# Kernel tuning notes

Hardware: AMD Instinct MI355X
Metric: run time of the kernel (lower is better)

Reference implementation:

```python
import jax, jax.numpy as jnp
import numpy as np

HEADS = 16
DIM_HEAD = 64


def setup_inputs() -> dict:
    key = jax.random.key(0)
    k1, k2, k3, k4 = jax.random.split(key, 4)
    B, T, D = 4, 1024, 1024
    x = jax.random.normal(k1, (B, T, D), dtype=jnp.float32)
    w_qkv = jax.random.normal(k2, (3 * HEADS * DIM_HEAD, D), dtype=jnp.float32) * (1.0 / np.sqrt(D))
    w_out = jax.random.normal(k3, (D, HEADS * DIM_HEAD), dtype=jnp.float32) * (1.0 / np.sqrt(HEADS * DIM_HEAD))
    rel_bias = jax.random.normal(k4, (2 * 1024 - 1, HEADS), dtype=jnp.float32) * 0.02
    return {"x": x, "w_qkv": w_qkv, "w_out": w_out, "rel_bias": rel_bias}


def reference(x, w_qkv, w_out, rel_bias):
    b, t, _ = x.shape
    h, dh = HEADS, DIM_HEAD
    scale = dh ** (-0.5)
    qkv = x @ w_qkv.T  # [b, t, 3*h*dh]
    # einops 'b t (d k h) -> k b h t d': last axis factors as (dh, 3, h)
    qkv = qkv.reshape(b, t, dh, 3, h).transpose(3, 0, 4, 1, 2)  # [3, b, h, t, dh]
    q, k, v = qkv[0], qkv[1], qkv[2]
    scores = jnp.einsum('bhid,bhjd->bhij', q, k) * scale  # [b, h, t, t]
    # relative position bias: rel[i,j] = j - i + t - 1
    rel = jnp.arange(t)[None, :] - jnp.arange(t)[:, None] + (t - 1)  # [t, t]
    bias = rel_bias[rel]  # [t, t, h]
    scores = scores + bias.transpose(2, 0, 1)[None]  # [b, h, t, t]
    attn = jax.nn.softmax(scores, axis=-1)
    out = jnp.einsum('bhij,bhjd->bhid', attn, v)  # [b, h, t, dh]
    out = out.transpose(0, 2, 1, 3).reshape(b, t, h * dh)  # 'b h t d -> b t (h d)'
    return out @ w_out.T
```

## Files before the change

### kernel.cpp

```cpp
#include <hip/hip_runtime.h>
#include <hip/hip_bf16.h>

typedef short bf16x8 __attribute__((ext_vector_type(8)));
typedef float f32x4  __attribute__((ext_vector_type(4)));

typedef __attribute__((address_space(3))) void lds_t;
typedef __attribute__((address_space(1))) void gbl_t;

#define MFMA16(a,b,c) __builtin_amdgcn_mfma_f32_16x16x32_bf16((a),(b),(c),0,0,0)

__device__ __forceinline__ unsigned short f2bf(float f) {
    __hip_bfloat16 h = __float2bfloat16(f);
    return __builtin_bit_cast(unsigned short, h);
}
__device__ __forceinline__ float bf2f(unsigned short u) {
    __hip_bfloat16 h = __builtin_bit_cast(__hip_bfloat16, u);
    return __bfloat162float(h);
}

__global__ void prep_hi_rows(const float* __restrict__ src,
                             unsigned short* __restrict__ dst, int total4) {
    for (int idx = blockIdx.x * blockDim.x + threadIdx.x; idx < total4;
         idx += gridDim.x * blockDim.x) {
        int base = idx * 4;
        float4 v = *reinterpret_cast<const float4*>(src + base);
        ushort4 hi;
        hi.x = f2bf(v.x);
        hi.y = f2bf(v.y);
        hi.z = f2bf(v.z);
        hi.w = f2bf(v.w);
        *reinterpret_cast<ushort4*>(dst + base) = hi;
    }
}

__global__ void prep_hi_wqkv(const float* __restrict__ w,
                             unsigned short* __restrict__ dst) {
    for (int idx = blockIdx.x * blockDim.x + threadIdx.x; idx < 3072 * 256;
         idx += gridDim.x * blockDim.x) {
        int base = idx * 4;
        int n = base >> 10, c = base & 1023;
        int d = n & 63, which = n >> 10, h = (n >> 6) & 15;
        int srow = d * 48 + which * 16 + h;
        float4 v = *reinterpret_cast<const float4*>(w + (size_t)srow * 1024 + c);
        ushort4 hi;
        hi.x = f2bf(v.x);
        hi.y = f2bf(v.y);
        hi.z = f2bf(v.z);
        hi.w = f2bf(v.w);
        *reinterpret_cast<ushort4*>(dst + (size_t)n * 1024 + c) = hi;
    }
}

__global__ __launch_bounds__(512, 2) void gemm256_hi(
    const unsigned short* __restrict__ A, const unsigned short* __restrict__ B,
    unsigned short* __restrict__ outQ, unsigned short* __restrict__ outK,
    unsigned short* __restrict__ outV) {
    __shared__ unsigned short lds[65536];
    const int tid = threadIdx.x;
    const int wid = tid >> 6, lane = tid & 63;
    const int lrow = lane & 15, lgrp = lane >> 4;
    const int wr = wid >> 2, wc = wid & 3;
    const int mtile = blockIdx.y * 256, ntile = blockIdx.x * 256;

    const int csw = lgrp ^ ((lrow >> 1) & 3);
    const int aoff = (wr * 128 + lrow) * 32 + csw * 8;
    const int boff = 32768 + (wc * 64 + lrow) * 32 + csw * 8;

    const int sreg = wid * 2;
    const int srow0 = sreg * 16 + (lane >> 2);
    const int srow1 = (sreg + 1) * 16 + (lane >> 2);
    const int schunk = (lane & 3) ^ ((lane >> 3) & 3);
    const int sdst0 = sreg * 512;

    f32x4 acc[8][4];
#pragma unroll
    for (int i = 0; i < 8; ++i)
#pragma unroll
        for (int j = 0; j < 4; ++j) {
            f32x4 z = {0.f, 0.f, 0.f, 0.f};
            acc[i][j] = z;
        }

#pragma unroll
    for (int s0 = 0; s0 < 2; ++s0) {
        const int kb = s0 * 32;
        __builtin_amdgcn_global_load_lds(
            (const gbl_t*)(A + (size_t)(mtile + srow0) * 1024 + kb + schunk * 8),
            (lds_t*)(lds + s0 * 8192 + sdst0), 16, 0, 0);
        __builtin_amdgcn_global_load_lds(
            (const gbl_t*)(A + (size_t)(mtile + srow1) * 1024 + kb + schunk * 8),
            (lds_t*)(lds + s0 * 8192 + sdst0 + 512), 16, 0, 0);
        __builtin_amdgcn_global_load_lds(
            (const gbl_t*)(B + (size_t)(ntile + srow0) * 1024 + kb + schunk * 8),
            (lds_t*)(lds + 32768 + s0 * 8192 + sdst0), 16, 0, 0);
        __builtin_amdgcn_global_load_lds(
            (const gbl_t*)(B + (size_t)(ntile + srow1) * 1024 + kb + schunk * 8),
            (lds_t*)(lds + 32768 + s0 * 8192 + sdst0 + 512), 16, 0, 0);
    }
    asm volatile("s_waitcnt vmcnt(4)" ::: "memory");
    __syncthreads();

    for (int s = 0; s < 32; ++s) {
        const int sa = s & 3;
        const unsigned short* sbase = lds + sa * 8192;

        bf16x8 af[8];
#pragma unroll
        for (int i = 0; i < 8; ++i)
            af[i] = *reinterpret_cast<const bf16x8*>(sbase + aoff + i * 512);
        bf16x8 b0 = *reinterpret_cast<const bf16x8*>(sbase + boff);
        bf16x8 b1 = *reinterpret_cast<const bf16x8*>(sbase + boff + 512);

        if (s <= 29) {
            const int kb2 = (s + 2) * 32;
            const int s2 = (s + 2) & 3;
            __builtin_amdgcn_global_load_lds(
                (const gbl_t*)(A + (size_t)(mtile + srow0) * 1024 + kb2 + schunk * 8),
                (lds_t*)(lds + s2 * 8192 + sdst0), 16, 0, 0);
            __builtin_amdgcn_global_load_lds(
                (const gbl_t*)(A + (size_t)(mtile + srow1) * 1024 + kb2 + schunk * 8),
                (lds_t*)(lds + s2 * 8192 + sdst0 + 512), 16, 0, 0);
        }
        __builtin_amdgcn_s_setprio(1);
#pragma unroll
        for (int i = 0; i < 8; ++i) {
            acc[i][0] = MFMA16(af[i], b0, acc[i][0]);
            acc[i][1] = MFMA16(af[i], b1, acc[i][1]);
        }
        __builtin_amdgcn_s_setprio(0);

        bf16x8 b2 = *reinterpret_cast<const bf16x8*>(sbase + boff + 1024);
        bf16x8 b3 = *reinterpret_cast<const bf16x8*>(sbase + boff + 1536);
        if (s <= 29) {
            const int kb2 = (s + 2) * 32;
            const int s2 = (s + 2) & 3;
            __builtin_amdgcn_global_load_lds(
                (const gbl_t*)(B + (size_t)(ntile + srow0) * 1024 + kb2 + schunk * 8),
                (lds_t*)(lds + 32768 + s2 * 8192 + sdst0), 16, 0, 0);
            __builtin_amdgcn_global_load_lds(
                (const gbl_t*)(B + (size_t)(ntile + srow1) * 1024 + kb2 + schunk * 8),
                (lds_t*)(lds + 32768 + s2 * 8192 + sdst0 + 512), 16, 0, 0);
        }
        __builtin_amdgcn_s_setprio(1);
#pragma unroll
        for (int i = 0; i < 8; ++i) {
            acc[i][2] = MFMA16(af[i], b2, acc[i][2]);
            acc[i][3] = MFMA16(af[i], b3, acc[i][3]);
        }
        __builtin_amdgcn_s_setprio(0);

        if (s < 31) {
            if (s <= 29)
                asm volatile("s_waitcnt vmcnt(4)" ::: "memory");
            else
                asm volatile("s_waitcnt vmcnt(0)" ::: "memory");
            __syncthreads();
        }
    }

#pragma unroll
    for (int i = 0; i < 8; ++i) {
#pragma unroll
        for (int j = 0; j < 4; ++j) {
#pragma unroll
            for (int r = 0; r < 4; ++r) {
                float v = acc[i][j][r];
                int m = mtile + wr * 128 + i * 16 + lgrp * 4 + r;
                int n = ntile + wc * 64 + j * 16 + lrow;
                int which = n >> 10;
                int hh = (n >> 6) & 15;
                int d = n & 63;
                int b = m >> 10, t = m & 1023;
                unsigned short* dstp =
                    (which == 0) ? outQ : ((which == 1) ? outK : outV);
                dstp[((size_t)((b << 4) + hh) * 1024 + t) * 64 + d] = f2bf(v);
            }
        }
    }
}

__global__ __launch_bounds__(256, 3) void gemm_out_v4(
    const unsigned short* __restrict__ A, const unsigned short* __restrict__ B,
    float* __restrict__ outF) {
    __shared__ unsigned short As[4][64 * 32];
    __shared__ unsigned short Bs[4][128 * 32];
    const int tid = threadIdx.x;
    const int wid = tid >> 6, lane = tid & 63;
    const int lrow = lane & 15, lgrp = lane >> 4;
    const int wr = wid >> 1, wc = wid & 1;
    const int h = blockIdx.x;
    const int xcd = h & 7, within = h >> 3;
    const int mtile = (xcd * 8 + (within & 7)) * 64;
    const int ntile = (within >> 3) * 128;

    const int csw = lgrp ^ ((lrow >> 1) & 3);
    const int aoff = (wr * 32 + lrow) * 32 + csw * 8;
    const int boff = (wc * 64 + lrow) * 32 + csw * 8;

    const int srow = tid >> 2;
    const int schunk = (tid & 3) ^ ((tid >> 3) & 3);
    const unsigned short* Arow = A + (size_t)(mtile + srow) * 1024 + schunk * 8;
    const unsigned short* Brow0 = B + (size_t)(ntile + srow) * 1024 + schunk * 8;
    const unsigned short* Brow1 =
        B + (size_t)(ntile + 64 + srow) * 1024 + schunk * 8;

    f32x4 acc[2][4];
#pragma unroll
    for (int i = 0; i < 2; ++i)
#pragma unroll
        for (int j = 0; j < 4; ++j) {
            f32x4 z = {0.f, 0.f, 0.f, 0.f};
            acc[i][j] = z;
        }

#pragma unroll
    for (int s0 = 0; s0 < 2; ++s0) {
        const int kb = s0 * 32;
        __builtin_amdgcn_global_load_lds((const gbl_t*)(Arow + kb),
                                         (lds_t*)(&As[s0][0] + tid * 8), 16, 0,
                                         0);
        __builtin_amdgcn_global_load_lds((const gbl_t*)(Brow0 + kb),
                                         (lds_t*)(&Bs[s0][0] + tid * 8), 16, 0,
                                         0);
        __builtin_amdgcn_global_load_lds((const gbl_t*)(Brow1 + kb),
                                         (lds_t*)(&Bs[s0][0] + 2048 + tid * 8),
                                         16, 0, 0);
    }
    asm volatile("s_waitcnt vmcnt(3)" ::: "memory");
    __syncthreads();

    for (int s = 0; s < 32; ++s) {
        const int sa = s & 3;
        if (s <= 29) {
            const int kb = (s + 2) * 32;
            const int s2 = (s + 2) & 3;
            __builtin_amdgcn_global_load_lds((const gbl_t*)(Arow + kb),
                                             (lds_t*)(&As[s2][0] + tid * 8), 16,
                                             0, 0);
            __builtin_amdgcn_global_load_lds((const gbl_t*)(Brow0 + kb),
                                             (lds_t*)(&Bs[s2][0] + tid * 8), 16,
                                             0, 0);
            __builtin_amdgcn_global_load_lds(
                (const gbl_t*)(Brow1 + kb),
                (lds_t*)(&Bs[s2][0] + 2048 + tid * 8), 16, 0, 0);
        }
        bf16x8 af[2], bfv[4];
#pragma unroll
        for (int i = 0; i < 2; ++i)
            af[i] = *reinterpret_cast<const bf16x8*>(&As[sa][0] + aoff + i * 512);
#pragma unroll
        for (int j = 0; j < 4; ++j)
            bfv[j] =
                *reinterpret_cast<const bf16x8*>(&Bs[sa][0] + boff + j * 512);
        __builtin_amdgcn_s_setprio(1);
#pragma unroll
        for (int i = 0; i < 2; ++i)
#pragma unroll
            for (int j = 0; j < 4; ++j)
                acc[i][j] = MFMA16(af[i], bfv[j], acc[i][j]);
        __builtin_amdgcn_s_setprio(0);
        if (s < 31) {
            if (s <= 29)
                asm volatile("s_waitcnt vmcnt(3)" ::: "memory");
            else
                asm volatile("s_waitcnt vmcnt(0)" ::: "memory");
            __syncthreads();
        }
    }

#pragma unroll
    for (int i = 0; i < 2; ++i)
#pragma unroll
        for (int j = 0; j < 4; ++j)
#pragma unroll
            for (int r = 0; r < 4; ++r) {
                int m = mtile + wr * 32 + i * 16 + lgrp * 4 + r;
                int n = ntile + wc * 64 + j * 16 + lrow;
                outF[(size_t)m * 1024 + n] = acc[i][j][r];
            }
}

__global__ __launch_bounds__(256) void transpose_v(
    const unsigned short* __restrict__ Vb, unsigned short* __restrict__ Vtg) {
    __shared__ unsigned short L[64][72];
    const int tt = blockIdx.x, bh = blockIdx.y;
    const int tid = threadIdx.x;
#pragma unroll
    for (int e = 0; e < 2; ++e) {
        int chunk = e * 256 + tid;
        int r = chunk >> 3, c = (chunk & 7) * 8;
        uint4 v = *reinterpret_cast<const uint4*>(
            Vb + ((size_t)bh * 1024 + tt * 64 + r) * 64 + c);
        *reinterpret_cast<uint4*>(&L[r][c]) = v;
    }
    __syncthreads();
#pragma unroll
    for (int e = 0; e < 2; ++e) {
        int chunk = e * 256 + tid;
        int d = chunk >> 3, t0 = (chunk & 7) * 8;
        unsigned short tmp[8];
#pragma unroll
        for (int u = 0; u < 8; ++u) tmp[u] = L[t0 + u][d];
        *reinterpret_cast<uint4*>(Vtg + ((size_t)bh * 64 + d) * 1024 + tt * 64 +
                                  t0) = *reinterpret_cast<const uint4*>(tmp);
    }
}

__global__ __launch_bounds__(512) void attn_kernel(
    const unsigned short* __restrict__ Qb, const unsigned short* __restrict__ Kb,
    const unsigned short* __restrict__ Vtg, const float* __restrict__ rel_bias,
    unsigned short* __restrict__ A3) {
    const int qt = blockIdx.x;
    const int bh = blockIdx.y;
    const int b = bh >> 4, h = bh & 15;
    const int tid = threadIdx.x;
    const int w = tid >> 6, lane = tid & 63;
    const int lrow = lane & 15, lgrp = lane >> 4;
    const float LOG2E = 1.4426950408889634f;
    const float SCALE2 = 0.125f * 1.4426950408889634f;
    const float THR = 11.5f;

    __shared__ unsigned short Ks[2][64 * 64];
    __shared__ unsigned short Vs[2][64 * 64];
    __shared__ unsigned short Ps[8][16 * 64];
    __shared__ float Bias2[2][192];

    const unsigned short* Ktile = Kb + (size_t)bh * 1024 * 64;
    const unsigned short* Vtile = Vtg + (size_t)bh * 64 * 1024;

    const unsigned short* Qp =
        Qb + ((size_t)bh * 1024 + qt * 128 + w * 16 + lrow) * 64;
    bf16x8 qa0 = *reinterpret_cast<const bf16x8*>(Qp + lgrp * 8);
    bf16x8 qa1 = *reinterpret_cast<const bf16x8*>(Qp + 32 + lgrp * 8);

    const int sr0 = w * 8 + (lane >> 3);
    const int sc_lo = lane & 7;

    float m_run = -3.0e38f;
    float l_run = 0.f;
    f32x4 o_acc[4];
#pragma unroll
    for (int n = 0; n < 4; n++) {
        f32x4 z = {0.f, 0.f, 0.f, 0.f};
        o_acc[n] = z;
    }

    const int bbase = lgrp * 4 + 127 - w * 16 - lrow;

    {
        {
            int r = sr0;
            int c = sc_lo ^ (r & 7);
            __builtin_amdgcn_global_load_lds(
                (const gbl_t*)(Ktile + (size_t)r * 64 + c * 8),
                (lds_t*)(&Ks[0][0] + w * 512), 16, 0, 0);
            __builtin_amdgcn_global_load_lds(
                (const gbl_t*)(Vtile + (size_t)r * 1024 + c * 8),
                (lds_t*)(&Vs[0][0] + w * 512), 16, 0, 0);
        }
        if (tid < 192) {
            int rowi = 0 - qt * 128 + 896 + tid;
            rowi = (rowi < 2046) ? rowi : 2046;
            Bias2[0][tid] = rel_bias[(size_t)rowi * 16 + h] * LOG2E;
        }
        asm volatile("s_waitcnt vmcnt(0)" ::: "memory");
        __syncthreads();
    }

    for (int kv = 0; kv < 16; ++kv) {
        const int cur = kv & 1;
        if (kv < 15) {
            const int j0n = (kv + 1) * 64;
            int r = sr0;
            int c = sc_lo ^ (r & 7);
            __builtin_amdgcn_global_load_lds(
                (const gbl_t*)(Ktile + (size_t)(j0n + r) * 64 + c * 8),
                (lds_t*)(&Ks[cur ^ 1][0] + w * 512), 16, 0, 0);
            __builtin_amdgcn_global_load_lds(
                (const gbl_t*)(Vtile + (size_t)r * 1024 + j0n + c * 8),
                (lds_t*)(&Vs[cur ^ 1][0] + w * 512), 16, 0, 0);
            if (tid < 192) {
                int rowi = j0n - qt * 128 + 896 + tid;
                rowi = (rowi < 2046) ? rowi : 2046;
                Bias2[cur ^ 1][tid] = rel_bias[(size_t)rowi * 16 + h] * LOG2E;
            }
        }

        const unsigned short* kbuf = &Ks[cur][0];
        f32x4 s[4];
        __builtin_amdgcn_s_setprio(1);
#pragma unroll
        for (int f = 0; f < 4; ++f) {
            int krow = f * 16 + lrow;
            int sw0 = (lgrp ^ (lrow & 7)) * 8;
            int sw1 = ((4 | lgrp) ^ (lrow & 7)) * 8;
            bf16x8 kb0 = *reinterpret_cast<const bf16x8*>(kbuf + krow * 64 + sw0);
            bf16x8 kb1 = *reinterpret_cast<const bf16x8*>(kbuf + krow * 64 + sw1);
            f32x4 z = {0.f, 0.f, 0.f, 0.f};
            z = MFMA16(kb0, qa0, z);
            z = MFMA16(kb1, qa1, z);
            s[f] = z;
        }
        __builtin_amdgcn_s_setprio(0);

        float x[4][4];
        float pm = -3.0e38f;
#pragma unroll
        for (int f = 0; f < 4; ++f)
#pragma unroll
            for (int r = 0; r < 4; ++r) {
                float xv = s[f][r] * SCALE2 + Bias2[cur][bbase + f * 16 + r];
                x[f][r] = xv;
                pm = fmaxf(pm, xv);
            }
        pm = fmaxf(pm, __shfl_xor(pm, 16));
        pm = fmaxf(pm, __shfl_xor(pm, 32));

        if (!__all(pm - m_run <= THR)) {
            float mnew = fmaxf(m_run, pm);
            float corr = __builtin_amdgcn_exp2f(m_run - mnew);
            m_run = mnew;
            l_run *= corr;
            float cb[4];
#pragma unroll
            for (int r = 0; r < 4; ++r) cb[r] = __shfl(corr, lgrp * 4 + r);
#pragma unroll
            for (int n = 0; n < 4; n++)
#pragma unroll
                for (int r = 0; r < 4; r++) o_acc[n][r] *= cb[r];
        }

        float su = 0.f;
#pragma unroll
        for (int f = 0; f < 4; ++f)
#pragma unroll
            for (int r = 0; r < 4; ++r) {
                float pv = __builtin_amdgcn_exp2f(x[f][r] - m_run);
                x[f][r] = pv;
                su += pv;
            }
        l_run += su;

#pragma unroll
        for (int f = 0; f < 4; ++f) {
            unsigned int plo, phi;
            asm("v_cvt_pk_bf16_f32 %0, %1, %2"
                : "=v"(plo)
                : "v"(x[f][0]), "v"(x[f][1]));
            asm("v_cvt_pk_bf16_f32 %0, %1, %2"
                : "=v"(phi)
                : "v"(x[f][2]), "v"(x[f][3]));
            const int chunk = (f * 2 + (lgrp >> 1)) ^ (lrow & 7);
            uint2 pw;
            pw.x = plo;
            pw.y = phi;
            *reinterpret_cast<uint2*>(
                &Ps[w][lrow * 64 + chunk * 8 + (lgrp & 1) * 4]) = pw;
        }

        const unsigned short* vbuf = &Vs[cur][0];
        __builtin_amdgcn_s_setprio(1);
#pragma unroll
        for (int jc = 0; jc < 2; ++jc) {
            int pc = ((4 * jc + lgrp) ^ (lrow & 7)) * 8;
            bf16x8 pa =
                *reinterpret_cast<const bf16x8*>(&Ps[w][0] + lrow * 64 + pc);
#pragma unroll
            for (int n = 0; n < 4; n++) {
                int vrow = n * 16 + lrow;
                bf16x8 vb =
                    *reinterpret_cast<const bf16x8*>(vbuf + vrow * 64 + pc);
                o_acc[n] = MFMA16(pa, vb, o_acc[n]);
            }
        }
        __builtin_amdgcn_s_setprio(0);

        if (kv < 15) {
            asm volatile("s_waitcnt vmcnt(0)" ::: "memory");
            __syncthreads();
        }
    }

    float lt = l_run + __shfl_xor(l_run, 16);
    lt += __shfl_xor(lt, 32);
    float rl[4];
#pragma unroll
    for (int r = 0; r < 4; ++r) rl[r] = 1.0f / __shfl(lt, lgrp * 4 + r);

#pragma unroll
    for (int n = 0; n < 4; n++) {
#pragma unroll
        for (int r = 0; r < 4; r++) {
            float val = o_acc[n][r] * rl[r];
            int ia = qt * 128 + w * 16 + lgrp * 4 + r;
            size_t m = (size_t)b * 1024 + ia;
            int col = h * 64 + n * 16 + lrow;
            A3[m * 1024 + col] = f2bf(val);
        }
    }
}

extern "C" void kernel_launch(void* const* d_in, const int* in_sizes, int n_in,
                              void* d_out, int out_size, void* d_ws,
                              size_t ws_size, hipStream_t stream) {
    const float* x = (const float*)d_in[0];
    const float* w_qkv = (const float*)d_in[1];
    const float* w_out = (const float*)d_in[2];
    const float* rel_bias = (const float*)d_in[3];
    float* out = (float*)d_out;

    char* ws = (char*)d_ws;
    size_t off = 0;
    auto alloc = [&](size_t bytes) {
        char* p = ws + off;
        off += (bytes + 255) & ~(size_t)255;
        return p;
    };
    unsigned short* A1h = (unsigned short*)alloc((size_t)4096 * 1024 * 2);
    unsigned short* W1h = (unsigned short*)alloc((size_t)3072 * 1024 * 2);
    unsigned short* Qb = (unsigned short*)alloc((size_t)64 * 1024 * 64 * 2);
    unsigned short* Kb = (unsigned short*)alloc((size_t)64 * 1024 * 64 * 2);
    unsigned short* Vb = (unsigned short*)alloc((size_t)64 * 1024 * 64 * 2);
    unsigned short* A3h = (unsigned short*)alloc((size_t)4096 * 1024 * 2);
    unsigned short* W3h = (unsigned short*)alloc((size_t)1024 * 1024 * 2);
    unsigned short* Vtg = A1h;

    hipLaunchKernelGGL(prep_hi_rows, dim3(1024), dim3(256), 0, stream, x, A1h,
                       4096 * 256);
    hipLaunchKernelGGL(prep_hi_wqkv, dim3(768), dim3(256), 0, stream, w_qkv,
                       W1h);
    hipLaunchKernelGGL(prep_hi_rows, dim3(256), dim3(256), 0, stream, w_out,
                       W3h, 1024 * 256);
    hipLaunchKernelGGL(gemm256_hi, dim3(12, 16), dim3(512), 0, stream, A1h, W1h,
                       Qb, Kb, Vb);
    hipLaunchKernelGGL(transpose_v, dim3(16, 64), dim3(256), 0, stream, Vb, Vtg);
    hipLaunchKernelGGL(attn_kernel, dim3(8, 64), dim3(512), 0, stream, Qb, Kb,
                       Vtg, rel_bias, A3h);
    hipLaunchKernelGGL(gemm_out_v4, dim3(512), dim3(256), 0, stream, A3h, W3h,
                       out);
}
```

Measured before the change: 113.1 us.

## Shrink QKV GEMM tile to 128x256, 3-stage LDS, write V transposed directly

The QKV projection GEMM now uses a 128x256 tile with a three-stage LDS ring instead of 256x256 with four stages. That doubles the grid to 384 blocks and allows more blocks per CU, so the 256 CUs are better filled. The GEMM epilogue writes V directly in the transposed [bh][d][t] layout, which removes the separate transpose_v kernel and its extra global round trip. The transposed store writes with stride along t per lane, so V writes are less coalesced, and smaller tiles lower the arithmetic reuse per block.

```diff
diff --git a/kernel.cpp b/kernel.cpp
--- a/kernel.cpp
+++ b/kernel.cpp
@@ -51,30 +51,31 @@
     }
 }
 
-__global__ __launch_bounds__(512, 2) void gemm256_hi(
+__global__ __launch_bounds__(512, 4) void gemm256_hi(
     const unsigned short* __restrict__ A, const unsigned short* __restrict__ B,
     unsigned short* __restrict__ outQ, unsigned short* __restrict__ outK,
-    unsigned short* __restrict__ outV) {
-    __shared__ unsigned short lds[65536];
+    unsigned short* __restrict__ outVt) {
+    __shared__ unsigned short lds[3 * 12288];
     const int tid = threadIdx.x;
     const int wid = tid >> 6, lane = tid & 63;
     const int lrow = lane & 15, lgrp = lane >> 4;
     const int wr = wid >> 2, wc = wid & 3;
-    const int mtile = blockIdx.y * 256, ntile = blockIdx.x * 256;
+    const int mtile = blockIdx.y * 128, ntile = blockIdx.x * 256;
 
     const int csw = lgrp ^ ((lrow >> 1) & 3);
-    const int aoff = (wr * 128 + lrow) * 32 + csw * 8;
-    const int boff = 32768 + (wc * 64 + lrow) * 32 + csw * 8;
-
-    const int sreg = wid * 2;
-    const int srow0 = sreg * 16 + (lane >> 2);
-    const int srow1 = (sreg + 1) * 16 + (lane >> 2);
-    const int schunk = (lane & 3) ^ ((lane >> 3) & 3);
-    const int sdst0 = sreg * 512;
-
-    f32x4 acc[8][4];
-#pragma unroll
-    for (int i = 0; i < 8; ++i)
+    const int aoff = (wr * 64 + lrow) * 32 + csw * 8;
+    const int boff = 4096 + (wc * 64 + lrow) * 32 + csw * 8;
+
+    const int srow = tid >> 2;
+    const int schunk = (tid & 3) ^ ((tid >> 3) & 3);
+    const unsigned short* Arow = A + (size_t)(mtile + srow) * 1024 + schunk * 8;
+    const unsigned short* Brow0 = B + (size_t)(ntile + srow) * 1024 + schunk * 8;
+    const unsigned short* Brow1 =
+        B + (size_t)(ntile + 128 + srow) * 1024 + schunk * 8;
+
+    f32x4 acc[4][4];
+#pragma unroll
+    for (int i = 0; i < 4; ++i)
 #pragma unroll
         for (int j = 0; j < 4; ++j) {
             f32x4 z = {0.f, 0.f, 0.f, 0.f};
@@ -84,96 +85,84 @@
 #pragma unroll
     for (int s0 = 0; s0 < 2; ++s0) {
         const int kb = s0 * 32;
+        __builtin_amdgcn_global_load_lds((const gbl_t*)(Arow + kb),
+                                         (lds_t*)(lds + s0 * 12288 + tid * 8),
+                                         16, 0, 0);
         __builtin_amdgcn_global_load_lds(
-            (const gbl_t*)(A + (size_t)(mtile + srow0) * 1024 + kb + schunk * 8),
-            (lds_t*)(lds + s0 * 8192 + sdst0), 16, 0, 0);
+            (const gbl_t*)(Brow0 + kb),
+            (lds_t*)(lds + s0 * 12288 + 4096 + tid * 8), 16, 0, 0);
         __builtin_amdgcn_global_load_lds(
-            (const gbl_t*)(A + (size_t)(mtile + srow1) * 1024 + kb + schunk * 8),
-            (lds_t*)(lds + s0 * 8192 + sdst0 + 512), 16, 0, 0);
-        __builtin_amdgcn_global_load_lds(
-            (const gbl_t*)(B + (size_t)(ntile + srow0) * 1024 + kb + schunk * 8),
-            (lds_t*)(lds + 32768 + s0 * 8192 + sdst0), 16, 0, 0);
-        __builtin_amdgcn_global_load_lds(
-            (const gbl_t*)(B + (size_t)(ntile + srow1) * 1024 + kb + schunk * 8),
-            (lds_t*)(lds + 32768 + s0 * 8192 + sdst0 + 512), 16, 0, 0);
-    }
-    asm volatile("s_waitcnt vmcnt(4)" ::: "memory");
+            (const gbl_t*)(Brow1 + kb),
+            (lds_t*)(lds + s0 * 12288 + 8192 + tid * 8), 16, 0, 0);
+    }
+    asm volatile("s_waitcnt vmcnt(3)" ::: "memory");
     __syncthreads();
 
+    int sa = 0;
     for (int s = 0; s < 32; ++s) {
-        const int sa = s & 3;
-        const unsigned short* sbase = lds + sa * 8192;
-
-        bf16x8 af[8];
-#pragma unroll
-        for (int i = 0; i < 8; ++i)
+        const unsigned short* sbase = lds + sa * 12288;
+
+        bf16x8 af[4], bfv[4];
+#pragma unroll
+        for (int i = 0; i < 4; ++i)
             af[i] = *reinterpret_cast<const bf16x8*>(sbase + aoff + i * 512);
-        bf16x8 b0 = *reinterpret_cast<const bf16x8*>(sbase + boff);
-        bf16x8 b1 = *reinterpret_cast<const bf16x8*>(sbase + boff + 512);
+#pragma unroll
+        for (int j = 0; j < 4; ++j)
+            bfv[j] = *reinterpret_cast<const bf16x8*>(sbase + boff + j * 512);
 
         if (s <= 29) {
-            const int kb2 = (s + 2) * 32;
-            const int s2 = (s + 2) & 3;
-            __builtin_amdgcn_global_load_lds(
-                (const gbl_t*)(A + (size_t)(mtile + srow0) * 1024 + kb2 + schunk * 8),
-                (lds_t*)(lds + s2 * 8192 + sdst0), 16, 0, 0);
-            __builtin_amdgcn_global_load_lds(
-                (const gbl_t*)(A + (size_t)(mtile + srow1) * 1024 + kb2 + schunk * 8),
-                (lds_t*)(lds + s2 * 8192 + sdst0 + 512), 16, 0, 0);
+            int s2 = sa + 2;
+            if (s2 >= 3) s2 -= 3;
+            const int kb = (s + 2) * 32;
+            __builtin_amdgcn_global_load_lds(
+                (const gbl_t*)(Arow + kb), (lds_t*)(lds + s2 * 12288 + tid * 8),
+                16, 0, 0);
+            __builtin_amdgcn_global_load_lds(
+                (const gbl_t*)(Brow0 + kb),
+                (lds_t*)(lds + s2 * 12288 + 4096 + tid * 8), 16, 0, 0);
+            __builtin_amdgcn_global_load_lds(
+                (const gbl_t*)(Brow1 + kb),
+                (lds_t*)(lds + s2 * 12288 + 8192 + tid * 8), 16, 0, 0);
         }
         __builtin_amdgcn_s_setprio(1);
 #pragma unroll
-        for (int i = 0; i < 8; ++i) {
-            acc[i][0] = MFMA16(af[i], b0, acc[i][0]);
-            acc[i][1] = MFMA16(af[i], b1, acc[i][1]);
-        }
-        __builtin_amdgcn_s_setprio(0);
-
-        bf16x8 b2 = *reinterpret_cast<const bf16x8*>(sbase + boff + 1024);
-        bf16x8 b3 = *reinterpret_cast<const bf16x8*>(sbase + boff + 1536);
-        if (s <= 29) {
-            const int kb2 = (s + 2) * 32;
-            const int s2 = (s + 2) & 3;
-            __builtin_amdgcn_global_load_lds(
-                (const gbl_t*)(B + (size_t)(ntile + srow0) * 1024 + kb2 + schunk * 8),
-                (lds_t*)(lds + 32768 + s2 * 8192 + sdst0), 16, 0, 0);
-            __builtin_amdgcn_global_load_lds(
-                (const gbl_t*)(B + (size_t)(ntile + srow1) * 1024 + kb2 + schunk * 8),
-                (lds_t*)(lds + 32768 + s2 * 8192 + sdst0 + 512), 16, 0, 0);
-        }
-        __builtin_amdgcn_s_setprio(1);
-#pragma unroll
-        for (int i = 0; i < 8; ++i) {
-            acc[i][2] = MFMA16(af[i], b2, acc[i][2]);
-            acc[i][3] = MFMA16(af[i], b3, acc[i][3]);
-        }
+        for (int i = 0; i < 4; ++i)
+#pragma unroll
+            for (int j = 0; j < 4; ++j)
+                acc[i][j] = MFMA16(af[i], bfv[j], acc[i][j]);
         __builtin_amdgcn_s_setprio(0);
 
         if (s < 31) {
             if (s <= 29)
-                asm volatile("s_waitcnt vmcnt(4)" ::: "memory");
+                asm volatile("s_waitcnt vmcnt(3)" ::: "memory");
             else
                 asm volatile("s_waitcnt vmcnt(0)" ::: "memory");
             __syncthreads();
         }
-    }
-
-#pragma unroll
-    for (int i = 0; i < 8; ++i) {
+        sa = (sa + 1 == 3) ? 0 : sa + 1;
+    }
+
+#pragma unroll
+    for (int i = 0; i < 4; ++i) {
 #pragma unroll
         for (int j = 0; j < 4; ++j) {
 #pragma unroll
             for (int r = 0; r < 4; ++r) {
                 float v = acc[i][j][r];
-                int m = mtile + wr * 128 + i * 16 + lgrp * 4 + r;
+                int m = mtile + wr * 64 + i * 16 + lgrp * 4 + r;
                 int n = ntile + wc * 64 + j * 16 + lrow;
                 int which = n >> 10;
                 int hh = (n >> 6) & 15;
                 int d = n & 63;
                 int b = m >> 10, t = m & 1023;
-                unsigned short* dstp =
-                    (which == 0) ? outQ : ((which == 1) ? outK : outV);
-                dstp[((size_t)((b << 4) + hh) * 1024 + t) * 64 + d] = f2bf(v);
+                if (which == 2) {
+                    outVt[((size_t)((b << 4) + hh) * 64 + d) * 1024 + t] =
+                        f2bf(v);
+                } else {
+                    unsigned short* dstp = (which == 0) ? outQ : outK;
+                    dstp[((size_t)((b << 4) + hh) * 1024 + t) * 64 + d] =
+                        f2bf(v);
+                }
             }
         }
     }
@@ -278,32 +267,6 @@
                 int n = ntile + wc * 64 + j * 16 + lrow;
                 outF[(size_t)m * 1024 + n] = acc[i][j][r];
             }
-}
-
-__global__ __launch_bounds__(256) void transpose_v(
-    const unsigned short* __restrict__ Vb, unsigned short* __restrict__ Vtg) {
-    __shared__ unsigned short L[64][72];
-    const int tt = blockIdx.x, bh = blockIdx.y;
-    const int tid = threadIdx.x;
-#pragma unroll
-    for (int e = 0; e < 2; ++e) {
-        int chunk = e * 256 + tid;
-        int r = chunk >> 3, c = (chunk & 7) * 8;
-        uint4 v = *reinterpret_cast<const uint4*>(
-            Vb + ((size_t)bh * 1024 + tt * 64 + r) * 64 + c);
-        *reinterpret_cast<uint4*>(&L[r][c]) = v;
-    }
-    __syncthreads();
-#pragma unroll
-    for (int e = 0; e < 2; ++e) {
-        int chunk = e * 256 + tid;
-        int d = chunk >> 3, t0 = (chunk & 7) * 8;
-        unsigned short tmp[8];
-#pragma unroll
-        for (int u = 0; u < 8; ++u) tmp[u] = L[t0 + u][d];
-        *reinterpret_cast<uint4*>(Vtg + ((size_t)bh * 64 + d) * 1024 + tt * 64 +
-                                  t0) = *reinterpret_cast<const uint4*>(tmp);
-    }
 }
 
 __global__ __launch_bounds__(512) void attn_kernel(
@@ -520,10 +483,9 @@
     unsigned short* W1h = (unsigned short*)alloc((size_t)3072 * 1024 * 2);
     unsigned short* Qb = (unsigned short*)alloc((size_t)64 * 1024 * 64 * 2);
     unsigned short* Kb = (unsigned short*)alloc((size_t)64 * 1024 * 64 * 2);
-    unsigned short* Vb = (unsigned short*)alloc((size_t)64 * 1024 * 64 * 2);
+    unsigned short* Vtg = (unsigned short*)alloc((size_t)64 * 64 * 1024 * 2);
     unsigned short* A3h = (unsigned short*)alloc((size_t)4096 * 1024 * 2);
     unsigned short* W3h = (unsigned short*)alloc((size_t)1024 * 1024 * 2);
-    unsigned short* Vtg = A1h;
 
     hipLaunchKernelGGL(prep_hi_rows, dim3(1024), dim3(256), 0, stream, x, A1h,
                        4096 * 256);
@@ -531,9 +493,8 @@
                        W1h);
     hipLaunchKernelGGL(prep_hi_rows, dim3(256), dim3(256), 0, stream, w_out,
                        W3h, 1024 * 256);
-    hipLaunchKernelGGL(gemm256_hi, dim3(12, 16), dim3(512), 0, stream, A1h, W1h,
-                       Qb, Kb, Vb);
-    hipLaunchKernelGGL(transpose_v, dim3(16, 64), dim3(256), 0, stream, Vb, Vtg);
+    hipLaunchKernelGGL(gemm256_hi, dim3(12, 32), dim3(512), 0, stream, A1h, W1h,
+                       Qb, Kb, Vtg);
     hipLaunchKernelGGL(attn_kernel, dim3(8, 64), dim3(512), 0, stream, Qb, Kb,
                        Vtg, rel_bias, A3h);
     hipLaunchKernelGGL(gemm_out_v4, dim3(512), dim3(256), 0, stream, A3h, W3h,
```

Measured after the change: 118.0 us. +4.4%, slower.

## Read K/V fragments directly from global memory and preload full bias window

Applied to the files above, without the earlier changes.

Removes the double-buffered LDS staging of K and V tiles and the per-iteration barriers, so each wave loads its MFMA operands straight from global memory (relying on L1/L2 caching, since all 8 waves read the same K/V). The per-tile bias staging is replaced by a single preload of the whole 1151-entry bias window into shared memory at kernel start. This cuts LDS traffic and synchronisation but duplicates global/L2 reads across waves and exposes global load latency directly in the MFMA loop without explicit prefetch.

```diff
diff --git a/kernel.cpp b/kernel.cpp
--- a/kernel.cpp
+++ b/kernel.cpp
@@ -320,10 +320,8 @@
     const float SCALE2 = 0.125f * 1.4426950408889634f;
     const float THR = 11.5f;
 
-    __shared__ unsigned short Ks[2][64 * 64];
-    __shared__ unsigned short Vs[2][64 * 64];
     __shared__ unsigned short Ps[8][16 * 64];
-    __shared__ float Bias2[2][192];
+    __shared__ float BiasF[1152];
 
     const unsigned short* Ktile = Kb + (size_t)bh * 1024 * 64;
     const unsigned short* Vtile = Vtg + (size_t)bh * 64 * 1024;
@@ -333,9 +331,6 @@
     bf16x8 qa0 = *reinterpret_cast<const bf16x8*>(Qp + lgrp * 8);
     bf16x8 qa1 = *reinterpret_cast<const bf16x8*>(Qp + 32 + lgrp * 8);
 
-    const int sr0 = w * 8 + (lane >> 3);
-    const int sc_lo = lane & 7;
-
     float m_run = -3.0e38f;
     float l_run = 0.f;
     f32x4 o_acc[4];
@@ -345,57 +340,26 @@
         o_acc[n] = z;
     }
 
+    {
+        const int rbase = 896 - qt * 128;
+        for (int t = tid; t < 1151; t += 512)
+            BiasF[t] = rel_bias[(size_t)(t + rbase) * 16 + h] * LOG2E;
+        __syncthreads();
+    }
+
     const int bbase = lgrp * 4 + 127 - w * 16 - lrow;
 
-    {
-        {
-            int r = sr0;
-            int c = sc_lo ^ (r & 7);
-            __builtin_amdgcn_global_load_lds(
-                (const gbl_t*)(Ktile + (size_t)r * 64 + c * 8),
-                (lds_t*)(&Ks[0][0] + w * 512), 16, 0, 0);
-            __builtin_amdgcn_global_load_lds(
-                (const gbl_t*)(Vtile + (size_t)r * 1024 + c * 8),
-                (lds_t*)(&Vs[0][0] + w * 512), 16, 0, 0);
-        }
-        if (tid < 192) {
-            int rowi = 0 - qt * 128 + 896 + tid;
-            rowi = (rowi < 2046) ? rowi : 2046;
-            Bias2[0][tid] = rel_bias[(size_t)rowi * 16 + h] * LOG2E;
-        }
-        asm volatile("s_waitcnt vmcnt(0)" ::: "memory");
-        __syncthreads();
-    }
-
     for (int kv = 0; kv < 16; ++kv) {
-        const int cur = kv & 1;
-        if (kv < 15) {
-            const int j0n = (kv + 1) * 64;
-            int r = sr0;
-            int c = sc_lo ^ (r & 7);
-            __builtin_amdgcn_global_load_lds(
-                (const gbl_t*)(Ktile + (size_t)(j0n + r) * 64 + c * 8),
-                (lds_t*)(&Ks[cur ^ 1][0] + w * 512), 16, 0, 0);
-            __builtin_amdgcn_global_load_lds(
-                (const gbl_t*)(Vtile + (size_t)r * 1024 + j0n + c * 8),
-                (lds_t*)(&Vs[cur ^ 1][0] + w * 512), 16, 0, 0);
-            if (tid < 192) {
-                int rowi = j0n - qt * 128 + 896 + tid;
-                rowi = (rowi < 2046) ? rowi : 2046;
-                Bias2[cur ^ 1][tid] = rel_bias[(size_t)rowi * 16 + h] * LOG2E;
-            }
-        }
-
-        const unsigned short* kbuf = &Ks[cur][0];
+        const int j0 = kv * 64;
+
         f32x4 s[4];
         __builtin_amdgcn_s_setprio(1);
 #pragma unroll
         for (int f = 0; f < 4; ++f) {
-            int krow = f * 16 + lrow;
-            int sw0 = (lgrp ^ (lrow & 7)) * 8;
-            int sw1 = ((4 | lgrp) ^ (lrow & 7)) * 8;
-            bf16x8 kb0 = *reinterpret_cast<const bf16x8*>(kbuf + krow * 64 + sw0);
-            bf16x8 kb1 = *reinterpret_cast<const bf16x8*>(kbuf + krow * 64 + sw1);
+            const unsigned short* krp =
+                Ktile + (size_t)(j0 + f * 16 + lrow) * 64 + lgrp * 8;
+            bf16x8 kb0 = *reinterpret_cast<const bf16x8*>(krp);
+            bf16x8 kb1 = *reinterpret_cast<const bf16x8*>(krp + 32);
             f32x4 z = {0.f, 0.f, 0.f, 0.f};
             z = MFMA16(kb0, qa0, z);
             z = MFMA16(kb1, qa1, z);
@@ -409,7 +373,7 @@
         for (int f = 0; f < 4; ++f)
 #pragma unroll
             for (int r = 0; r < 4; ++r) {
-                float xv = s[f][r] * SCALE2 + Bias2[cur][bbase + f * 16 + r];
+                float xv = s[f][r] * SCALE2 + BiasF[j0 + bbase + f * 16 + r];
                 x[f][r] = xv;
                 pm = fmaxf(pm, xv);
             }
@@ -458,7 +422,6 @@
                 &Ps[w][lrow * 64 + chunk * 8 + (lgrp & 1) * 4]) = pw;
         }
 
-        const unsigned short* vbuf = &Vs[cur][0];
         __builtin_amdgcn_s_setprio(1);
 #pragma unroll
         for (int jc = 0; jc < 2; ++jc) {
@@ -467,18 +430,14 @@
                 *reinterpret_cast<const bf16x8*>(&Ps[w][0] + lrow * 64 + pc);
 #pragma unroll
             for (int n = 0; n < 4; n++) {
-                int vrow = n * 16 + lrow;
-                bf16x8 vb =
-                    *reinterpret_cast<const bf16x8*>(vbuf + vrow * 64 + pc);
+                const unsigned short* vrp = Vtile +
+                                            (size_t)(n * 16 + lrow) * 1024 + j0 +
+                                            jc * 32 + lgrp * 8;
+                bf16x8 vb = *reinterpret_cast<const bf16x8*>(vrp);
                 o_acc[n] = MFMA16(pa, vb, o_acc[n]);
             }
         }
         __builtin_amdgcn_s_setprio(0);
-
-        if (kv < 15) {
-            asm volatile("s_waitcnt vmcnt(0)" ::: "memory");
-            __syncthreads();
-        }
     }
 
     float lt = l_run + __shfl_xor(l_run, 16);
```

After: 194.4 us. 1.72x slower.
